# Optimization experiments

Measured on AMD Instinct MI355X. Metric: run time of the kernel, lower is better.

The kernel has to match this reference:

```python
import jax, jax.numpy as jnp
import numpy as np
import math

LN_EPS = 1e-5

def layer_norm(x, g, b):
    mu = jnp.mean(x, axis=-1, keepdims=True)
    var = jnp.mean(jnp.square(x - mu), axis=-1, keepdims=True)
    return (x - mu) * jax.lax.rsqrt(var + LN_EPS) * g + b

def positional_encoding(seq_len, d_model):
    pos = jnp.arange(seq_len, dtype=jnp.float32)[:, None]
    div = jnp.exp(jnp.arange(0, d_model, 2, dtype=jnp.float32) * (-math.log(10000.0) / d_model))
    ang = pos * div  # [S, D/2]
    # interleave: even indices sin, odd indices cos
    return jnp.stack([jnp.sin(ang), jnp.cos(ang)], axis=-1).reshape(seq_len, d_model)

def setup_inputs() -> dict:
    key = jax.random.key(0)
    V, D, H, L, F, B, S = 32000, 768, 12, 6, 3072, 4, 1024
    ks = jax.random.split(key, 12)
    s = 0.02
    inp = {
        'tokens': jax.random.randint(ks[0], (B, S), 0, V),
        'emb': jax.random.normal(ks[1], (V, D), jnp.float32) * s,
        'Wq': jax.random.normal(ks[2], (L, D, D), jnp.float32) * s,
        'bq': jnp.zeros((L, D), jnp.float32),
        'Wk': jax.random.normal(ks[3], (L, D, D), jnp.float32) * s,
        'bk': jnp.zeros((L, D), jnp.float32),
        'Wv': jax.random.normal(ks[4], (L, D, D), jnp.float32) * s,
        'bv': jnp.zeros((L, D), jnp.float32),
        'Wo': jax.random.normal(ks[5], (L, D, D), jnp.float32) * s,
        'bo': jnp.zeros((L, D), jnp.float32),
        'W1': jax.random.normal(ks[6], (L, D, F), jnp.float32) * s,
        'b1': jnp.zeros((L, F), jnp.float32),
        'W2': jax.random.normal(ks[7], (L, F, D), jnp.float32) * s,
        'b2': jnp.zeros((L, D), jnp.float32),
        'ln1_g': jnp.ones((L, D), jnp.float32), 'ln1_b': jnp.zeros((L, D), jnp.float32),
        'ln2_g': jnp.ones((L, D), jnp.float32), 'ln2_b': jnp.zeros((L, D), jnp.float32),
        'lnf_g': jnp.ones((D,), jnp.float32), 'lnf_b': jnp.zeros((D,), jnp.float32),
        'head_W': jax.random.normal(ks[8], (V, D), jnp.float32) * s,
    }
    return inp

def gpt_forward(tokens, emb, Wq, bq, Wk, bk, Wv, bv, Wo, bo, W1, b1, W2, b2,
                ln1_g, ln1_b, ln2_g, ln2_b, lnf_g, lnf_b, head_W):
    B, S = tokens.shape
    D = emb.shape[1]
    H = 12
    dk = D // H
    scale = 1.0 / math.sqrt(dk)
    causal = jnp.tril(jnp.ones((S, S), dtype=bool))  # [S,S]

    x = emb[tokens] + positional_encoding(S, D)  # [B,S,D]

    def block(x, p):
        wq, bq_, wk, bk_, wv, bv_, wo, bo_, w1, b1_, w2, b2_, g1, be1, g2, be2 = p
        h = layer_norm(x, g1, be1)
        q = (h @ wq + bq_).reshape(B, S, H, dk)
        k = (h @ wk + bk_).reshape(B, S, H, dk)
        v = (h @ wv + bv_).reshape(B, S, H, dk)
        scores = jnp.einsum('bqhd,bkhd->bhqk', q, k) * scale
        scores = jnp.where(causal, scores, -jnp.inf)
        attn = jax.nn.softmax(scores, axis=-1)
        o = jnp.einsum('bhqk,bkhd->bqhd', attn, v).reshape(B, S, D)
        x = x + o @ wo + bo_
        h2 = layer_norm(x, g2, be2)
        ff = jax.nn.gelu(h2 @ w1 + b1_, approximate=False) @ w2 + b2_
        x = x + ff
        return x, None

    layer_params = (Wq, bq, Wk, bk, Wv, bv, Wo, bo, W1, b1, W2, b2,
                    ln1_g, ln1_b, ln2_g, ln2_b)
    x, _ = jax.lax.scan(block, x, layer_params)
    x = layer_norm(x, lnf_g, lnf_b)
    logits = jnp.einsum('bsd,vd->bsv', x, head_W)  # head bias=False
    return logits

def reference(tokens, emb, Wq, bq, Wk, bk, Wv, bv, Wo, bo, W1, b1, W2, b2,
              ln1_g, ln1_b, ln2_g, ln2_b, lnf_g, lnf_b, head_W):
    return gpt_forward(tokens, emb, Wq, bq, Wk, bk, Wv, bv, Wo, bo, W1, b1, W2, b2,
                       ln1_g, ln1_b, ln2_g, ln2_b, lnf_g, lnf_b, head_W)
```

## Files before the change

kernel.cpp:

```cpp
#include <hip/hip_runtime.h>
#include <hip/hip_bf16.h>
#include <math.h>

#define BB 4
#define SS 1024
#define DD 768
#define HH 12
#define LL 6
#define FF 3072
#define VV 32000
#define DK 64
#define MM (BB * SS)

typedef __attribute__((ext_vector_type(8))) short s8v;
typedef __attribute__((ext_vector_type(4))) float f4v;

__device__ inline unsigned short f2bf_bits(float f) {
    unsigned u = __builtin_bit_cast(unsigned, f);
    unsigned r = (u + 0x7fffu + ((u >> 16) & 1u)) >> 16;
    return (unsigned short)r;
}

__device__ inline void gl_lds16(const void* g, void* l) {
    __builtin_amdgcn_global_load_lds((const __attribute__((address_space(1))) void*)g,
                                     (__attribute__((address_space(3))) void*)l, 16, 0, 0);
}

__global__ void embed_kernel(const int* __restrict__ tokens,
                             const float* __restrict__ emb,
                             float* __restrict__ x) {
    const int row = blockIdx.x;
    const int s = row % SS;
    const int tok = tokens[row];
    const float* er = emb + (size_t)tok * DD;
    float* xr = x + (size_t)row * DD;
    const float neg_ln_base = -logf(10000.0f) / (float)DD;
    for (int d = threadIdx.x; d < DD; d += blockDim.x) {
        int i2 = d & ~1;
        float div = expf((float)i2 * neg_ln_base);
        float ang = (float)s * div;
        float pe = (d & 1) ? cosf(ang) : sinf(ang);
        xr[d] = er[d] + pe;
    }
}

template <int OUTBF>
__global__ __launch_bounds__(256) void ln_kernel(const float* __restrict__ x,
                                                 const float* __restrict__ g,
                                                 const float* __restrict__ b,
                                                 void* __restrict__ outp) {
    const int row = blockIdx.x;
    const float* xr = x + (size_t)row * DD;
    float s = 0.f, s2 = 0.f;
    for (int d = threadIdx.x; d < DD; d += blockDim.x) {
        float v = xr[d];
        s += v; s2 += v * v;
    }
    __shared__ float rs[4], rs2[4];
    for (int off = 32; off; off >>= 1) {
        s  += __shfl_down(s, off);
        s2 += __shfl_down(s2, off);
    }
    const int wid = threadIdx.x >> 6;
    if ((threadIdx.x & 63) == 0) { rs[wid] = s; rs2[wid] = s2; }
    __syncthreads();
    s  = rs[0] + rs[1] + rs[2] + rs[3];
    s2 = rs2[0] + rs2[1] + rs2[2] + rs2[3];
    const float mu = s / (float)DD;
    const float var = s2 / (float)DD - mu * mu;
    const float r = rsqrtf(var + 1e-5f);
    for (int d = threadIdx.x; d < DD; d += blockDim.x) {
        float v = (xr[d] - mu) * r * g[d] + b[d];
        if (OUTBF) ((unsigned short*)outp)[(size_t)row * DD + d] = f2bf_bits(v);
        else       ((float*)outp)[(size_t)row * DD + d] = v;
    }
}

__global__ __launch_bounds__(256) void prep_kernel(const float* __restrict__ Wq,
                                                   const float* __restrict__ Wk,
                                                   const float* __restrict__ Wv,
                                                   const float* __restrict__ Wo,
                                                   const float* __restrict__ W1,
                                                   const float* __restrict__ W2,
                                                   unsigned short* __restrict__ wqkvT,
                                                   unsigned short* __restrict__ woT,
                                                   unsigned short* __restrict__ w1T,
                                                   unsigned short* __restrict__ w2T) {
    const size_t DxD = (size_t)DD * DD, DxF = (size_t)DD * FF;
    const int lid = blockIdx.x / 1728;
    const int id  = blockIdx.x % 1728;
    const float* src; unsigned short* dst; int R, C, t;
    if (id < 432)       { int seg = id / 144; t = id % 144;
                          src = (seg == 0 ? Wq : seg == 1 ? Wk : Wv) + lid * DxD;
                          dst = wqkvT + lid * 3 * DxD + (size_t)seg * DxD; R = DD; C = DD; }
    else if (id < 576)  { t = id - 432; src = Wo + lid * DxD; dst = woT + lid * DxD; R = DD; C = DD; }
    else if (id < 1152) { t = id - 576;  src = W1 + lid * DxF; dst = w1T + lid * DxF; R = DD; C = FF; }
    else                { t = id - 1152; src = W2 + lid * DxF; dst = w2T + lid * DxF; R = FF; C = DD; }
    const int tilesC = C / 64;
    const int r0 = (t / tilesC) * 64, c0 = (t % tilesC) * 64;
    __shared__ float tb[64][65];
    const int lr = threadIdx.x >> 6, lc = threadIdx.x & 63;
    #pragma unroll
    for (int it = 0; it < 16; ++it) {
        int r = it * 4 + lr;
        tb[r][lc] = src[(size_t)(r0 + r) * C + c0 + lc];
    }
    __syncthreads();
    #pragma unroll
    for (int it = 0; it < 16; ++it) {
        int c = it * 4 + lr;
        dst[(size_t)(c0 + c) * R + r0 + lc] = f2bf_bits(tb[lc][c]);
    }
}

__global__ __launch_bounds__(256) void conv_kernel(const float* __restrict__ in,
                                                   unsigned short* __restrict__ out,
                                                   long n4) {
    long i = (long)blockIdx.x * 256 + threadIdx.x;
    if (i < n4) {
        float4 v = ((const float4*)in)[i];
        ushort4 o;
        o.x = f2bf_bits(v.x); o.y = f2bf_bits(v.y);
        o.z = f2bf_bits(v.z); o.w = f2bf_bits(v.w);
        ((ushort4*)out)[i] = o;
    }
}

template <int BM, int BN, int WGM, int WGN, int ACT, int RES, int OUTMODE>
__global__ __launch_bounds__(256) void gemm_mfma(const unsigned short* __restrict__ A,
                                                 const unsigned short* __restrict__ Bt,
                                                 const float* __restrict__ bias,
                                                 const float* res,
                                                 void* Cout, int M, int N, int K,
                                                 const float* biasK, const float* biasV,
                                                 unsigned short* kout, unsigned short* vtout) {
    __shared__ unsigned short As[BM * 32];
    __shared__ unsigned short Bs[BN * 32];
    constexpr int MF = (BM / WGM) / 16;
    constexpr int NF = (BN / WGN) / 16;
    const int tid = threadIdx.x;
    const int bm = blockIdx.y * BM, bn = blockIdx.x * BN;
    const int lane = tid & 63;
    const int wave = tid >> 6;
    const int wr = (wave / WGN) * (BM / WGM);
    const int wc = (wave % WGN) * (BN / WGN);

    f4v acc[MF][NF];
    #pragma unroll
    for (int i = 0; i < MF; i++)
        #pragma unroll
        for (int j = 0; j < NF; j++)
            acc[i][j] = (f4v){0.f, 0.f, 0.f, 0.f};

    const int arow = tid >> 2;
    const int acol = (tid & 3) * 8;
    const int fr = lane & 15;
    const int fk = (lane >> 4) * 8;

    for (int k0 = 0; k0 < K; k0 += 32) {
        #pragma unroll
        for (int i = 0; i < BM / 64; i++)
            gl_lds16(A + (size_t)(bm + i * 64 + arow) * K + k0 + acol,
                     (char*)As + i * 4096 + tid * 16);
        #pragma unroll
        for (int i = 0; i < BN / 64; i++)
            gl_lds16(Bt + (size_t)(bn + i * 64 + arow) * K + k0 + acol,
                     (char*)Bs + i * 4096 + tid * 16);
        __syncthreads();
        s8v af[MF], bf[NF];
        #pragma unroll
        for (int i = 0; i < MF; i++)
            af[i] = *(const s8v*)(As + (wr + i * 16 + fr) * 32 + fk);
        #pragma unroll
        for (int j = 0; j < NF; j++)
            bf[j] = *(const s8v*)(Bs + (wc + j * 16 + fr) * 32 + fk);
        #pragma unroll
        for (int i = 0; i < MF; i++)
            #pragma unroll
            for (int j = 0; j < NF; j++)
                acc[i][j] = __builtin_amdgcn_mfma_f32_16x16x32_bf16(af[i], bf[j], acc[i][j], 0, 0, 0);
        __syncthreads();
    }

    const int r0 = bm + wr + (lane >> 4) * 4;
    const int c0 = bn + wc + fr;
    #pragma unroll
    for (int i = 0; i < MF; i++) {
        const int rb = r0 + i * 16;
        #pragma unroll
        for (int j = 0; j < NF; j++) {
            const int c = c0 + j * 16;
            if (OUTMODE == 3) {
                const int seg = (c >= 1536) ? 2 : (c >= 768 ? 1 : 0);
                const int cc = c - seg * 768;
                const float bb = (seg == 0 ? bias[cc] : seg == 1 ? biasK[cc] : biasV[cc]);
                if (seg < 2) {
                    unsigned short* dst = (seg == 0 ? (unsigned short*)Cout : kout);
                    #pragma unroll
                    for (int q = 0; q < 4; q++)
                        dst[(size_t)(rb + q) * DD + cc] = f2bf_bits(acc[i][j][q] + bb);
                } else {
                    const int b_ = rb / SS, s_ = rb % SS;
                    const int h_ = cc >> 6, dd = cc & 63;
                    ushort4 pk;
                    pk.x = f2bf_bits(acc[i][j][0] + bb);
                    pk.y = f2bf_bits(acc[i][j][1] + bb);
                    pk.z = f2bf_bits(acc[i][j][2] + bb);
                    pk.w = f2bf_bits(acc[i][j][3] + bb);
                    *(ushort4*)(vtout + ((size_t)(b_ * HH + h_) * DK + dd) * SS + s_) = pk;
                }
            } else {
                const float bv = bias ? bias[c] : 0.f;
                #pragma unroll
                for (int q = 0; q < 4; q++) {
                    const int r = rb + q;
                    float v = acc[i][j][q] + bv;
                    if (ACT) v = 0.5f * v * (1.0f + erff(v * 0.70710678118654752f));
                    if (RES) v += res[(size_t)r * N + c];
                    if (OUTMODE == 1) ((unsigned short*)Cout)[(size_t)r * N + c] = f2bf_bits(v);
                    else              ((float*)Cout)[(size_t)r * N + c] = v;
                }
            }
        }
    }
}

__global__ __launch_bounds__(512) void gemm_head(const unsigned short* __restrict__ A,
                                                 const unsigned short* __restrict__ Bt,
                                                 float* __restrict__ C,
                                                 int M, int N, int K) {
    __shared__ unsigned short As[256 * 32];
    __shared__ unsigned short Bs[128 * 32];
    const int tid = threadIdx.x;

    const int f = blockIdx.y * gridDim.x + blockIdx.x;
    const int cpx = (gridDim.x * gridDim.y) >> 3;
    const int virt = (f & 7) * cpx + (f >> 3);
    const int bx = virt / gridDim.y;
    const int by = virt % gridDim.y;
    const int bm = by * 256, bn = bx * 128;

    const int lane = tid & 63;
    const int wave = tid >> 6;
    const int wm = (wave >> 1) * 64;
    const int wn = (wave & 1) * 64;

    f4v acc[4][4];
    #pragma unroll
    for (int i = 0; i < 4; i++)
        #pragma unroll
        for (int j = 0; j < 4; j++)
            acc[i][j] = (f4v){0.f, 0.f, 0.f, 0.f};

    const int arow = tid >> 2;
    const int acol = (tid & 3) * 8;
    const unsigned short* gA0 = A  + (size_t)(bm + arow) * K + acol;
    const unsigned short* gA1 = gA0 + (size_t)128 * K;
    const unsigned short* gB  = Bt + (size_t)(bn + arow) * K + acol;
    char* lA0 = (char*)As + tid * 16;
    char* lA1 = lA0 + 8192;
    char* lB  = (char*)Bs + tid * 16;

    const int fr = lane & 15;
    const int fk = (lane >> 4) * 8;

    for (int k0 = 0; k0 < K; k0 += 32) {
        gl_lds16(gA0 + k0, lA0);
        gl_lds16(gA1 + k0, lA1);
        gl_lds16(gB + k0, lB);
        __syncthreads();
        s8v af[4], bf[4];
        #pragma unroll
        for (int i = 0; i < 4; i++)
            af[i] = *(const s8v*)(As + (wm + i * 16 + fr) * 32 + fk);
        #pragma unroll
        for (int j = 0; j < 4; j++)
            bf[j] = *(const s8v*)(Bs + (wn + j * 16 + fr) * 32 + fk);
        #pragma unroll
        for (int i = 0; i < 4; i++)
            #pragma unroll
            for (int j = 0; j < 4; j++)
                acc[i][j] = __builtin_amdgcn_mfma_f32_16x16x32_bf16(af[i], bf[j], acc[i][j], 0, 0, 0);
        __syncthreads();
    }

    const int r0 = bm + wm + (lane >> 4) * 4;
    const int c0 = bn + wn + fr;
    #pragma unroll
    for (int i = 0; i < 4; i++) {
        #pragma unroll
        for (int j = 0; j < 4; j++) {
            const int c = c0 + j * 16;
            #pragma unroll
            for (int q = 0; q < 4; q++) {
                const int r = r0 + i * 16 + q;
                __builtin_nontemporal_store(acc[i][j][q], &C[(size_t)r * N + c]);
            }
        }
    }
}

__global__ __launch_bounds__(256) void fattn_kernel(const unsigned short* __restrict__ qb,
                                                    const unsigned short* __restrict__ kb,
                                                    const unsigned short* __restrict__ vt,
                                                    unsigned short* __restrict__ o) {
    __shared__ unsigned short Ks[128 * 64];
    __shared__ unsigned short Vs[64 * 128];
    __shared__ unsigned short Ps[4][16 * 128];

    const int qt = (int)gridDim.x - 1 - (int)blockIdx.x;
    const int bh = blockIdx.y;
    const int b = bh / HH, h = bh % HH;
    const int tid = threadIdx.x;
    const int lane = tid & 63;
    const int w = tid >> 6;
    const int fr = lane & 15;
    const int g  = lane >> 4;

    const int krow_ = tid >> 3;
    const int kcol = ((tid & 7) ^ (krow_ & 7)) * 8;
    const int vrow_ = tid >> 4;
    const int vcol = ((tid & 15) ^ (vrow_ & 7)) * 8;

    const int q0w = qt * 128 + w * 32;
    s8v qf[2][2];
    #pragma unroll
    for (int ri = 0; ri < 2; ri++) {
        const unsigned short* qrow =
            qb + (size_t)(b * SS + q0w + ri * 16 + fr) * DD + h * DK + g * 8;
        qf[ri][0] = *(const s8v*)(qrow);
        qf[ri][1] = *(const s8v*)(qrow + 32);
    }

    f4v ofr[2][4];
    float mrow[2][4], lrow[2][4];
    #pragma unroll
    for (int ri = 0; ri < 2; ri++)
        #pragma unroll
        for (int z = 0; z < 4; z++) {
            ofr[ri][z] = (f4v){0.f, 0.f, 0.f, 0.f};
            mrow[ri][z] = -1e30f;
            lrow[ri][z] = 0.f;
        }

    unsigned short* Pw = &Ps[w][0];
    const int ktiles = qt + 1;

    for (int t = 0; t < ktiles; ++t) {
        const int k0 = t * 128;
        #pragma unroll
        for (int i = 0; i < 4; i++) {
            const int r = i * 32 + krow_;
            gl_lds16(kb + (size_t)(b * SS + k0 + r) * DD + h * DK + kcol,
                     (char*)Ks + i * 4096 + tid * 16);
        }
        #pragma unroll
        for (int i = 0; i < 4; i++) {
            const int d = i * 16 + vrow_;
            gl_lds16(vt + ((size_t)bh * DK + d) * SS + k0 + vcol,
                     (char*)Vs + i * 4096 + tid * 16);
        }
        __syncthreads();

        const bool diag = (t == qt);
        #pragma unroll
        for (int ri = 0; ri < 2; ri++) {
            float p[8][4];
            #pragma unroll
            for (int j = 0; j < 8; j++) {
                const char* kbase = (const char*)Ks + (j * 16 + fr) * 128;
                s8v b0 = *(const s8v*)(kbase + ((g * 16)      ^ ((fr & 7) << 4)));
                s8v b1 = *(const s8v*)(kbase + ((64 + g * 16) ^ ((fr & 7) << 4)));
                f4v a = (f4v){0.f, 0.f, 0.f, 0.f};
                a = __builtin_amdgcn_mfma_f32_16x16x32_bf16(qf[ri][0], b0, a, 0, 0, 0);
                a = __builtin_amdgcn_mfma_f32_16x16x32_bf16(qf[ri][1], b1, a, 0, 0, 0);
                #pragma unroll
                for (int pq = 0; pq < 4; pq++) {
                    float sv = a[pq] * 0.125f;
                    if (diag && (j * 16 + fr > w * 32 + ri * 16 + g * 4 + pq)) sv = -1e30f;
                    p[j][pq] = sv;
                }
            }

            float rmx[4];
            #pragma unroll
            for (int pq = 0; pq < 4; pq++) {
                float v0 = fmaxf(fmaxf(p[0][pq], p[1][pq]), fmaxf(p[2][pq], p[3][pq]));
                float v1 = fmaxf(fmaxf(p[4][pq], p[5][pq]), fmaxf(p[6][pq], p[7][pq]));
                rmx[pq] = fmaxf(v0, v1);
            }
            #pragma unroll
            for (int off = 1; off < 16; off <<= 1)
                #pragma unroll
                for (int pq = 0; pq < 4; pq++)
                    rmx[pq] = fmaxf(rmx[pq], __shfl_xor(rmx[pq], off));

            float mnew[4], scf[4], rsum[4];
            #pragma unroll
            for (int pq = 0; pq < 4; pq++) {
                mnew[pq] = fmaxf(mrow[ri][pq], rmx[pq]);
                scf[pq]  = __expf(mrow[ri][pq] - mnew[pq]);
                rsum[pq] = 0.f;
            }
            #pragma unroll
            for (int j = 0; j < 8; j++)
                #pragma unroll
                for (int pq = 0; pq < 4; pq++) {
                    float e = __expf(p[j][pq] - mnew[pq]);
                    p[j][pq] = e;
                    rsum[pq] += e;
                }
            #pragma unroll
            for (int off = 1; off < 16; off <<= 1)
                #pragma unroll
                for (int pq = 0; pq < 4; pq++)
                    rsum[pq] += __shfl_xor(rsum[pq], off);
            #pragma unroll
            for (int pq = 0; pq < 4; pq++) {
                lrow[ri][pq] = lrow[ri][pq] * scf[pq] + rsum[pq];
                mrow[ri][pq] = mnew[pq];
            }
            #pragma unroll
            for (int dj = 0; dj < 4; dj++)
                #pragma unroll
                for (int pq = 0; pq < 4; pq++)
                    ofr[ri][dj][pq] *= scf[pq];

            #pragma unroll
            for (int j = 0; j < 8; j++)
                #pragma unroll
                for (int pq = 0; pq < 4; pq++) {
                    const int r = g * 4 + pq;
                    *(unsigned short*)((char*)Pw + r * 256 +
                                       (((j * 16 + fr) * 2) ^ ((r & 7) << 4))) = f2bf_bits(p[j][pq]);
                }

            s8v pa[4];
            #pragma unroll
            for (int ks = 0; ks < 4; ks++)
                pa[ks] = *(const s8v*)((const char*)Pw + fr * 256 +
                                       ((ks * 64 + g * 16) ^ ((fr & 7) << 4)));
            #pragma unroll
            for (int dj = 0; dj < 4; dj++) {
                const char* vbase = (const char*)Vs + (dj * 16 + fr) * 256;
                #pragma unroll
                for (int ks = 0; ks < 4; ks++) {
                    s8v vv = *(const s8v*)(vbase + ((ks * 64 + g * 16) ^ ((fr & 7) << 4)));
                    ofr[ri][dj] = __builtin_amdgcn_mfma_f32_16x16x32_bf16(pa[ks], vv, ofr[ri][dj], 0, 0, 0);
                }
            }
        }
        __syncthreads();
    }

    #pragma unroll
    for (int ri = 0; ri < 2; ri++)
        #pragma unroll
        for (int pq = 0; pq < 4; pq++) {
            const float inv = 1.0f / lrow[ri][pq];
            const int row_abs = q0w + ri * 16 + g * 4 + pq;
            #pragma unroll
            for (int dj = 0; dj < 4; dj++)
                o[(size_t)(b * SS + row_abs) * DD + h * DK + dj * 16 + fr] =
                    f2bf_bits(ofr[ri][dj][pq] * inv);
        }
}

extern "C" void kernel_launch(void* const* d_in, const int* in_sizes, int n_in,
                              void* d_out, int out_size, void* d_ws, size_t ws_size,
                              hipStream_t stream) {
    const int*   tokens = (const int*)d_in[0];
    const float* emb    = (const float*)d_in[1];
    const float* Wq     = (const float*)d_in[2];
    const float* bq     = (const float*)d_in[3];
    const float* Wk     = (const float*)d_in[4];
    const float* bk     = (const float*)d_in[5];
    const float* Wv     = (const float*)d_in[6];
    const float* bv     = (const float*)d_in[7];
    const float* Wo     = (const float*)d_in[8];
    const float* bo     = (const float*)d_in[9];
    const float* W1     = (const float*)d_in[10];
    const float* b1     = (const float*)d_in[11];
    const float* W2     = (const float*)d_in[12];
    const float* b2     = (const float*)d_in[13];
    const float* ln1_g  = (const float*)d_in[14];
    const float* ln1_b  = (const float*)d_in[15];
    const float* ln2_g  = (const float*)d_in[16];
    const float* ln2_b  = (const float*)d_in[17];
    const float* lnf_g  = (const float*)d_in[18];
    const float* lnf_b  = (const float*)d_in[19];
    const float* headW  = (const float*)d_in[20];
    float* out = (float*)d_out;
    (void)in_sizes; (void)n_in; (void)out_size; (void)ws_size;

    const size_t MD  = (size_t)MM * DD;
    const size_t MF_ = (size_t)MM * FF;
    const size_t DxD = (size_t)DD * DD;
    const size_t DxF = (size_t)DD * FF;
    const size_t HWs = (size_t)VV * DD;

    char* p = (char*)d_ws;
    float*          x     = (float*)p;          p += MD * 4;
    unsigned short* qb    = (unsigned short*)p; p += MD * 2;
    unsigned short* kbuf  = (unsigned short*)p; p += MD * 2;
    unsigned short* vtb   = (unsigned short*)p; p += MD * 2;
    unsigned short* ao    = (unsigned short*)p; p += MD * 2;
    unsigned short* h     = (unsigned short*)p; p += MD * 2;
    unsigned short* mid   = (unsigned short*)p; p += MF_ * 2;
    unsigned short* wqkvT = (unsigned short*)p; p += 6 * 3 * DxD * 2;
    unsigned short* woT   = (unsigned short*)p; p += 6 * DxD * 2;
    unsigned short* w1T   = (unsigned short*)p; p += 6 * DxF * 2;
    unsigned short* w2T   = (unsigned short*)p; p += 6 * DxF * 2;
    unsigned short* hw    = (unsigned short*)p; p += HWs * 2;

    embed_kernel<<<MM, 256, 0, stream>>>(tokens, emb, x);
    conv_kernel<<<(int)((HWs / 4 + 255) / 256), 256, 0, stream>>>(headW, hw, (long)(HWs / 4));
    prep_kernel<<<6 * 1728, 256, 0, stream>>>(Wq, Wk, Wv, Wo, W1, W2, wqkvT, woT, w1T, w2T);

    const dim3 gQKV(2304 / 128, MM / 128);
    const dim3 gDn(DD / 64, MM / 128);
    const dim3 gF(FF / 128, MM / 128);
    const dim3 gHead(VV / 128, MM / 256);
    const dim3 gA(SS / 128, BB * HH);

    for (int l = 0; l < LL; l++) {
        ln_kernel<1><<<MM, 256, 0, stream>>>(x, ln1_g + l * DD, ln1_b + l * DD, h);
        gemm_mfma<128, 128, 2, 2, 0, 0, 3><<<gQKV, 256, 0, stream>>>(
            h, wqkvT + (size_t)l * 3 * DxD, bq + l * DD, nullptr, qb, MM, 2304, DD,
            bk + l * DD, bv + l * DD, kbuf, vtb);
        fattn_kernel<<<gA, 256, 0, stream>>>(qb, kbuf, vtb, ao);
        gemm_mfma<128, 64, 4, 1, 0, 1, 0><<<gDn, 256, 0, stream>>>(
            ao, woT + (size_t)l * DxD, bo + l * DD, x, x, MM, DD, DD,
            nullptr, nullptr, nullptr, nullptr);
        ln_kernel<1><<<MM, 256, 0, stream>>>(x, ln2_g + l * DD, ln2_b + l * DD, h);
        gemm_mfma<128, 128, 2, 2, 1, 0, 1><<<gF, 256, 0, stream>>>(
            h, w1T + (size_t)l * DxF, b1 + l * FF, nullptr, mid, MM, FF, DD,
            nullptr, nullptr, nullptr, nullptr);
        gemm_mfma<128, 64, 4, 1, 0, 1, 0><<<gDn, 256, 0, stream>>>(
            mid, w2T + (size_t)l * DxF, b2 + l * DD, x, x, MM, DD, FF,
            nullptr, nullptr, nullptr, nullptr);
    }

    ln_kernel<1><<<MM, 256, 0, stream>>>(x, lnf_g, lnf_b, h);
    gemm_head<<<gHead, 512, 0, stream>>>(h, hw, out, MM, VV, DD);
}
```

Baseline: 2.068 ms.

## Halve attention query tile, remap head GEMM blocks, widen down-proj GEMM tiles

Three separate changes. The flash-attention kernel now handles 64 query rows per block (16 per wave) instead of 128, which doubles the grid and shrinks causal load imbalance. The head GEMM swaps its generic XCD swizzle for a hardcoded mapping that groups blocks into 16-column bands for L2 reuse. The Wo and W2 GEMMs move from 128x64 to 128x128 tiles, giving fewer, larger blocks. Each block now reloads the full K/V tile for fewer query rows, and the head mapping depends on fixed grid sizes (250x16).

New measurement: 1.861 ms. -10.0%, faster.

```diff
diff --git a/kernel.cpp b/kernel.cpp
--- a/kernel.cpp
+++ b/kernel.cpp
@@ -234,10 +234,18 @@
     const int tid = threadIdx.x;
 
     const int f = blockIdx.y * gridDim.x + blockIdx.x;
-    const int cpx = (gridDim.x * gridDim.y) >> 3;
-    const int virt = (f & 7) * cpx + (f >> 3);
-    const int bx = virt / gridDim.y;
-    const int by = virt % gridDim.y;
+    const int v = (f & 7) * 500 + (f >> 3);
+    int bx, by;
+    if (v < 3840) {
+        const int bnd = v >> 8;
+        const int r = v & 255;
+        by = r >> 4;
+        bx = bnd * 16 + (r & 15);
+    } else {
+        const int r = v - 3840;
+        by = r / 10;
+        bx = 240 + r % 10;
+    }
     const int bm = by * 256, bn = bx * 128;
 
     const int lane = tid & 63;
@@ -322,29 +330,22 @@
     const int vrow_ = tid >> 4;
     const int vcol = ((tid & 15) ^ (vrow_ & 7)) * 8;
 
-    const int q0w = qt * 128 + w * 32;
-    s8v qf[2][2];
-    #pragma unroll
-    for (int ri = 0; ri < 2; ri++) {
-        const unsigned short* qrow =
-            qb + (size_t)(b * SS + q0w + ri * 16 + fr) * DD + h * DK + g * 8;
-        qf[ri][0] = *(const s8v*)(qrow);
-        qf[ri][1] = *(const s8v*)(qrow + 32);
-    }
-
-    f4v ofr[2][4];
-    float mrow[2][4], lrow[2][4];
-    #pragma unroll
-    for (int ri = 0; ri < 2; ri++)
-        #pragma unroll
-        for (int z = 0; z < 4; z++) {
-            ofr[ri][z] = (f4v){0.f, 0.f, 0.f, 0.f};
-            mrow[ri][z] = -1e30f;
-            lrow[ri][z] = 0.f;
-        }
+    const int q0w = qt * 64 + w * 16;
+    s8v qf[2];
+    {
+        const unsigned short* qrow = qb + (size_t)(b * SS + q0w + fr) * DD + h * DK + g * 8;
+        qf[0] = *(const s8v*)(qrow);
+        qf[1] = *(const s8v*)(qrow + 32);
+    }
+
+    f4v ofr[4];
+    #pragma unroll
+    for (int dj = 0; dj < 4; dj++) ofr[dj] = (f4v){0.f, 0.f, 0.f, 0.f};
+    float mrow[4] = {-1e30f, -1e30f, -1e30f, -1e30f};
+    float lrow[4] = {0.f, 0.f, 0.f, 0.f};
 
     unsigned short* Pw = &Ps[w][0];
-    const int ktiles = qt + 1;
+    const int ktiles = qt / 2 + 1;
 
     for (int t = 0; t < ktiles; ++t) {
         const int k0 = t * 128;
@@ -362,108 +363,103 @@
         }
         __syncthreads();
 
-        const bool diag = (t == qt);
-        #pragma unroll
-        for (int ri = 0; ri < 2; ri++) {
-            float p[8][4];
-            #pragma unroll
-            for (int j = 0; j < 8; j++) {
-                const char* kbase = (const char*)Ks + (j * 16 + fr) * 128;
-                s8v b0 = *(const s8v*)(kbase + ((g * 16)      ^ ((fr & 7) << 4)));
-                s8v b1 = *(const s8v*)(kbase + ((64 + g * 16) ^ ((fr & 7) << 4)));
-                f4v a = (f4v){0.f, 0.f, 0.f, 0.f};
-                a = __builtin_amdgcn_mfma_f32_16x16x32_bf16(qf[ri][0], b0, a, 0, 0, 0);
-                a = __builtin_amdgcn_mfma_f32_16x16x32_bf16(qf[ri][1], b1, a, 0, 0, 0);
-                #pragma unroll
-                for (int pq = 0; pq < 4; pq++) {
-                    float sv = a[pq] * 0.125f;
-                    if (diag && (j * 16 + fr > w * 32 + ri * 16 + g * 4 + pq)) sv = -1e30f;
-                    p[j][pq] = sv;
-                }
+        const bool diag = (t == ktiles - 1);
+        float p[8][4];
+        #pragma unroll
+        for (int j = 0; j < 8; j++) {
+            const char* kbase = (const char*)Ks + (j * 16 + fr) * 128;
+            s8v b0 = *(const s8v*)(kbase + ((g * 16)      ^ ((fr & 7) << 4)));
+            s8v b1 = *(const s8v*)(kbase + ((64 + g * 16) ^ ((fr & 7) << 4)));
+            f4v a = (f4v){0.f, 0.f, 0.f, 0.f};
+            a = __builtin_amdgcn_mfma_f32_16x16x32_bf16(qf[0], b0, a, 0, 0, 0);
+            a = __builtin_amdgcn_mfma_f32_16x16x32_bf16(qf[1], b1, a, 0, 0, 0);
+            #pragma unroll
+            for (int pq = 0; pq < 4; pq++) {
+                float sv = a[pq] * 0.125f;
+                if (diag && (k0 + j * 16 + fr > q0w + g * 4 + pq)) sv = -1e30f;
+                p[j][pq] = sv;
             }
-
-            float rmx[4];
+        }
+
+        float rmx[4];
+        #pragma unroll
+        for (int pq = 0; pq < 4; pq++) {
+            float v0 = fmaxf(fmaxf(p[0][pq], p[1][pq]), fmaxf(p[2][pq], p[3][pq]));
+            float v1 = fmaxf(fmaxf(p[4][pq], p[5][pq]), fmaxf(p[6][pq], p[7][pq]));
+            rmx[pq] = fmaxf(v0, v1);
+        }
+        #pragma unroll
+        for (int off = 1; off < 16; off <<= 1)
+            #pragma unroll
+            for (int pq = 0; pq < 4; pq++)
+                rmx[pq] = fmaxf(rmx[pq], __shfl_xor(rmx[pq], off));
+
+        float mnew[4], scf[4], rsum[4];
+        #pragma unroll
+        for (int pq = 0; pq < 4; pq++) {
+            mnew[pq] = fmaxf(mrow[pq], rmx[pq]);
+            scf[pq]  = __expf(mrow[pq] - mnew[pq]);
+            rsum[pq] = 0.f;
+        }
+        #pragma unroll
+        for (int j = 0; j < 8; j++)
             #pragma unroll
             for (int pq = 0; pq < 4; pq++) {
-                float v0 = fmaxf(fmaxf(p[0][pq], p[1][pq]), fmaxf(p[2][pq], p[3][pq]));
-                float v1 = fmaxf(fmaxf(p[4][pq], p[5][pq]), fmaxf(p[6][pq], p[7][pq]));
-                rmx[pq] = fmaxf(v0, v1);
+                float e = __expf(p[j][pq] - mnew[pq]);
+                p[j][pq] = e;
+                rsum[pq] += e;
             }
-            #pragma unroll
-            for (int off = 1; off < 16; off <<= 1)
-                #pragma unroll
-                for (int pq = 0; pq < 4; pq++)
-                    rmx[pq] = fmaxf(rmx[pq], __shfl_xor(rmx[pq], off));
-
-            float mnew[4], scf[4], rsum[4];
+        #pragma unroll
+        for (int off = 1; off < 16; off <<= 1)
+            #pragma unroll
+            for (int pq = 0; pq < 4; pq++)
+                rsum[pq] += __shfl_xor(rsum[pq], off);
+        #pragma unroll
+        for (int pq = 0; pq < 4; pq++) {
+            lrow[pq] = lrow[pq] * scf[pq] + rsum[pq];
+            mrow[pq] = mnew[pq];
+        }
+        #pragma unroll
+        for (int dj = 0; dj < 4; dj++)
+            #pragma unroll
+            for (int pq = 0; pq < 4; pq++)
+                ofr[dj][pq] *= scf[pq];
+
+        #pragma unroll
+        for (int j = 0; j < 8; j++)
             #pragma unroll
             for (int pq = 0; pq < 4; pq++) {
-                mnew[pq] = fmaxf(mrow[ri][pq], rmx[pq]);
-                scf[pq]  = __expf(mrow[ri][pq] - mnew[pq]);
-                rsum[pq] = 0.f;
+                const int r = g * 4 + pq;
+                *(unsigned short*)((char*)Pw + r * 256 +
+                                   (((j * 16 + fr) * 2) ^ ((r & 7) << 4))) = f2bf_bits(p[j][pq]);
             }
-            #pragma unroll
-            for (int j = 0; j < 8; j++)
-                #pragma unroll
-                for (int pq = 0; pq < 4; pq++) {
-                    float e = __expf(p[j][pq] - mnew[pq]);
-                    p[j][pq] = e;
-                    rsum[pq] += e;
-                }
-            #pragma unroll
-            for (int off = 1; off < 16; off <<= 1)
-                #pragma unroll
-                for (int pq = 0; pq < 4; pq++)
-                    rsum[pq] += __shfl_xor(rsum[pq], off);
-            #pragma unroll
-            for (int pq = 0; pq < 4; pq++) {
-                lrow[ri][pq] = lrow[ri][pq] * scf[pq] + rsum[pq];
-                mrow[ri][pq] = mnew[pq];
+
+        s8v pa[4];
+        #pragma unroll
+        for (int ks = 0; ks < 4; ks++)
+            pa[ks] = *(const s8v*)((const char*)Pw + fr * 256 +
+                                   ((ks * 64 + g * 16) ^ ((fr & 7) << 4)));
+        #pragma unroll
+        for (int dj = 0; dj < 4; dj++) {
+            const char* vbase = (const char*)Vs + (dj * 16 + fr) * 256;
+            #pragma unroll
+            for (int ks = 0; ks < 4; ks++) {
+                s8v vv = *(const s8v*)(vbase + ((ks * 64 + g * 16) ^ ((fr & 7) << 4)));
+                ofr[dj] = __builtin_amdgcn_mfma_f32_16x16x32_bf16(pa[ks], vv, ofr[dj], 0, 0, 0);
             }
-            #pragma unroll
-            for (int dj = 0; dj < 4; dj++)
-                #pragma unroll
-                for (int pq = 0; pq < 4; pq++)
-                    ofr[ri][dj][pq] *= scf[pq];
-
-            #pragma unroll
-            for (int j = 0; j < 8; j++)
-                #pragma unroll
-                for (int pq = 0; pq < 4; pq++) {
-                    const int r = g * 4 + pq;
-                    *(unsigned short*)((char*)Pw + r * 256 +
-                                       (((j * 16 + fr) * 2) ^ ((r & 7) << 4))) = f2bf_bits(p[j][pq]);
-                }
-
-            s8v pa[4];
-            #pragma unroll
-            for (int ks = 0; ks < 4; ks++)
-                pa[ks] = *(const s8v*)((const char*)Pw + fr * 256 +
-                                       ((ks * 64 + g * 16) ^ ((fr & 7) << 4)));
-            #pragma unroll
-            for (int dj = 0; dj < 4; dj++) {
-                const char* vbase = (const char*)Vs + (dj * 16 + fr) * 256;
-                #pragma unroll
-                for (int ks = 0; ks < 4; ks++) {
-                    s8v vv = *(const s8v*)(vbase + ((ks * 64 + g * 16) ^ ((fr & 7) << 4)));
-                    ofr[ri][dj] = __builtin_amdgcn_mfma_f32_16x16x32_bf16(pa[ks], vv, ofr[ri][dj], 0, 0, 0);
-                }
-            }
         }
         __syncthreads();
     }
 
     #pragma unroll
-    for (int ri = 0; ri < 2; ri++)
-        #pragma unroll
-        for (int pq = 0; pq < 4; pq++) {
-            const float inv = 1.0f / lrow[ri][pq];
-            const int row_abs = q0w + ri * 16 + g * 4 + pq;
-            #pragma unroll
-            for (int dj = 0; dj < 4; dj++)
-                o[(size_t)(b * SS + row_abs) * DD + h * DK + dj * 16 + fr] =
-                    f2bf_bits(ofr[ri][dj][pq] * inv);
-        }
+    for (int pq = 0; pq < 4; pq++) {
+        const float inv = 1.0f / lrow[pq];
+        const int row_abs = q0w + g * 4 + pq;
+        #pragma unroll
+        for (int dj = 0; dj < 4; dj++)
+            o[(size_t)(b * SS + row_abs) * DD + h * DK + dj * 16 + fr] =
+                f2bf_bits(ofr[dj][pq] * inv);
+    }
 }
 
 extern "C" void kernel_launch(void* const* d_in, const int* in_sizes, int n_in,
@@ -518,10 +514,10 @@
     prep_kernel<<<6 * 1728, 256, 0, stream>>>(Wq, Wk, Wv, Wo, W1, W2, wqkvT, woT, w1T, w2T);
 
     const dim3 gQKV(2304 / 128, MM / 128);
-    const dim3 gDn(DD / 64, MM / 128);
+    const dim3 gD(DD / 128, MM / 128);
     const dim3 gF(FF / 128, MM / 128);
     const dim3 gHead(VV / 128, MM / 256);
-    const dim3 gA(SS / 128, BB * HH);
+    const dim3 gA(SS / 64, BB * HH);
 
     for (int l = 0; l < LL; l++) {
         ln_kernel<1><<<MM, 256, 0, stream>>>(x, ln1_g + l * DD, ln1_b + l * DD, h);
@@ -529,14 +525,14 @@
             h, wqkvT + (size_t)l * 3 * DxD, bq + l * DD, nullptr, qb, MM, 2304, DD,
             bk + l * DD, bv + l * DD, kbuf, vtb);
         fattn_kernel<<<gA, 256, 0, stream>>>(qb, kbuf, vtb, ao);
-        gemm_mfma<128, 64, 4, 1, 0, 1, 0><<<gDn, 256, 0, stream>>>(
+        gemm_mfma<128, 128, 2, 2, 0, 1, 0><<<gD, 256, 0, stream>>>(
             ao, woT + (size_t)l * DxD, bo + l * DD, x, x, MM, DD, DD,
             nullptr, nullptr, nullptr, nullptr);
         ln_kernel<1><<<MM, 256, 0, stream>>>(x, ln2_g + l * DD, ln2_b + l * DD, h);
         gemm_mfma<128, 128, 2, 2, 1, 0, 1><<<gF, 256, 0, stream>>>(
             h, w1T + (size_t)l * DxF, b1 + l * FF, nullptr, mid, MM, FF, DD,
             nullptr, nullptr, nullptr, nullptr);
-        gemm_mfma<128, 64, 4, 1, 0, 1, 0><<<gDn, 256, 0, stream>>>(
+        gemm_mfma<128, 128, 2, 2, 0, 1, 0><<<gD, 256, 0, stream>>>(
             mid, w2T + (size_t)l * DxF, b2 + l * DD, x, x, MM, DD, FF,
             nullptr, nullptr, nullptr, nullptr);
     }
```
